# Optimization experiments

Hardware: AMD Instinct MI355X
Metric: run time of the kernel (lower is better)

The kernel has to match this reference:

```python
import jax, jax.numpy as jnp
import numpy as np

ALPHA = 1.5  # entmax alpha (EntmaxBisect default behavior, exponent 1/(alpha-1)=2)
N_ITER = 50  # EntmaxBisect default number of bisection iterations


def entmax_bisect(x, alpha=ALPHA, n_iter=N_ITER):
    """Entmax via bisection along the last axis (Peters & Martins), matching
    the torch entmax.EntmaxBisect forward (with ensure_sum_one=True)."""
    d = x.shape[-1]
    xs = x * (alpha - 1.0)
    max_val = jnp.max(xs, axis=-1, keepdims=True)
    tau_lo = max_val - 1.0
    tau_hi = max_val - (1.0 / d) ** (alpha - 1.0)

    inv_am1 = 1.0 / (alpha - 1.0)  # = 2.0 for alpha=1.5

    def p(tau):
        return jnp.maximum(xs - tau, 0.0) ** inv_am1

    f_lo = jnp.sum(p(tau_lo), axis=-1, keepdims=True) - 1.0
    dm0 = tau_hi - tau_lo

    def body(i, carry):
        tau_lo, dm = carry
        dm = dm * 0.5
        tau_m = tau_lo + dm
        f_m = jnp.sum(p(tau_m), axis=-1, keepdims=True) - 1.0
        tau_lo = jnp.where(f_m * f_lo >= 0, tau_m, tau_lo)
        return (tau_lo, dm)

    tau_lo, dm = jax.lax.fori_loop(0, n_iter, body, (tau_lo, dm0))
    p_m = p(tau_lo + dm)
    return p_m / jnp.sum(p_m, axis=-1, keepdims=True)


def setup_inputs() -> dict:
    key = jax.random.key(0)
    k1, k2, k3, k4 = jax.random.split(key, 4)
    bsz, nfield, nemb = 2048, 128, 128
    nhead, nhid, d_k = 8, 64, 64

    def xavier(k, shape, gain=1.414):
        fan_in, fan_out = shape[-2], shape[-1]
        std = gain * np.sqrt(2.0 / (fan_in + fan_out))
        return jax.random.normal(k, shape, dtype=jnp.float32) * std

    return {
        "x": jax.random.normal(k1, (bsz, nfield, nemb), dtype=jnp.float32),
        "bilinear_w": xavier(k2, (nhead, nemb, d_k)),
        "query": xavier(k3, (nhead, nhid, d_k)),
        "values": xavier(k4, (nhead, nhid, nfield)),
    }


def reference(x, bilinear_w, query, values):
    # x: [b, f, x(=nemb)]; bilinear_w: [k, x, y(=d_k)]; query: [k, o(=nhid), y]
    d_k = bilinear_w.shape[-1]
    scale = d_k ** (-0.5)
    # einsum('bfx,kxy,koy->bkof') split into two contractions
    kx = jnp.einsum('bfx,kxy->bkfy', x, bilinear_w)            # [b,k,f,y]
    att_gates = jnp.einsum('bkfy,koy->bkof', kx, query) * scale  # [b,k,o,f]
    sparse_gates = entmax_bisect(att_gates)
    return sparse_gates * values[None]  # einsum('bkof,kof->bkof')
```

## Files before the change

kernel.cpp:

```cpp
#include <hip/hip_runtime.h>
#include <hip/hip_bf16.h>


using half8_t  = __attribute__((ext_vector_type(8))) _Float16;
using half4_t  = __attribute__((ext_vector_type(4))) _Float16;
using fp16x2   = __attribute__((ext_vector_type(2))) __fp16;
using floatx4  = __attribute__((ext_vector_type(4))) float;

#define NBIS 8

#if defined(__has_builtin)
#if __has_builtin(__builtin_amdgcn_fdot2)
#define HAS_FDOT2 1
#endif
#endif
#ifndef HAS_FDOT2
#define HAS_FDOT2 0
#endif

__device__ __forceinline__ float frcp(float x) {
#if __has_builtin(__builtin_amdgcn_rcpf)
    return __builtin_amdgcn_rcpf(x);
#else
    return 1.0f / x;
#endif
}

__global__ __launch_bounds__(256) void w2_kernel(const float* __restrict__ bw,
                                                 const float* __restrict__ qm,
                                                 _Float16* __restrict__ W2h) {
    const int k  = blockIdx.x >> 3;
    const int og = blockIdx.x & 7;
    __shared__ float Lbw[128 * 65];
    __shared__ float Lq[8 * 64];
    const int t = threadIdx.x;

    const float* bwk = bw + k * 8192;
    #pragma unroll
    for (int i2 = 0; i2 < 8; ++i2) {
        int i = t + i2 * 256;
        float4 v = ((const float4*)bwk)[i];
        int xx = (i * 4) >> 6, y = (i * 4) & 63;
        float* dst = &Lbw[xx * 65 + y];
        dst[0] = v.x; dst[1] = v.y; dst[2] = v.z; dst[3] = v.w;
    }
    const float* qk = qm + k * 4096 + og * 8 * 64;
    if (t < 128) ((float4*)Lq)[t] = ((const float4*)qk)[t];
    __syncthreads();

    #pragma unroll
    for (int i = 0; i < 4; ++i) {
        int ox = i * 256 + t;
        int o = ox >> 7, x = ox & 127;
        const float* brow = &Lbw[x * 65];
        const float* qrow = &Lq[o * 64];
        float acc = 0.f;
        #pragma unroll
        for (int y = 0; y < 64; ++y) acc = fmaf(brow[y], qrow[y], acc);
        W2h[(k * 64 + og * 8 + o) * 128 + x] = (_Float16)(acc * 0.0625f);
    }
}

__global__ __launch_bounds__(256, 3) void satt_kernel(
        const float* __restrict__ xg, const _Float16* __restrict__ W2h,
        const float* __restrict__ values, float* __restrict__ out) {
    const int bid = blockIdx.x;
    const int k = (bid & 511) >> 6;
    const int b = ((bid >> 9) << 6) | (bid & 63);
    const int t = threadIdx.x;
    const int w = t >> 6, l = t & 63;

    __shared__ __align__(16) char smem[52224];
    _Float16* Ash = (_Float16*)smem;
    _Float16* Bsh = (_Float16*)(smem + 17408);
    float*    zsh = (float*)smem;

    const _Float16* w2k = W2h + k * 8192;
    #pragma unroll
    for (int j = 0; j < 4; ++j) {
        int c = t + 256 * j;
        int o = c >> 4, x0 = (c & 15) * 8;
        uint4 v = ((const uint4*)w2k)[c];
        *(uint4*)(Ash + o * 136 + x0) = v;
    }
    const float* xb = xg + (size_t)b * 16384;
    #pragma unroll
    for (int j = 0; j < 16; ++j) {
        int c = t + 256 * j;
        int f = c >> 5, x0 = (c & 31) * 4;
        float4 v = ((const float4*)xb)[c];
        half4_t h;
        h[0] = (_Float16)v.x; h[1] = (_Float16)v.y;
        h[2] = (_Float16)v.z; h[3] = (_Float16)v.w;
        *(half4_t*)(Bsh + f * 136 + x0) = h;
    }
    __syncthreads();

    const int q = l >> 4, c16 = l & 15;
    half8_t afrag[4];
    #pragma unroll
    for (int kk = 0; kk < 4; ++kk)
        afrag[kk] = *(const half8_t*)(Ash + (w * 16 + c16) * 136 + kk * 32 + q * 8);

    floatx4 acc[8];
    #pragma unroll
    for (int ft = 0; ft < 8; ++ft) acc[ft] = (floatx4){0.f, 0.f, 0.f, 0.f};

    #pragma unroll
    for (int kk = 0; kk < 4; ++kk) {
        #pragma unroll
        for (int ft = 0; ft < 8; ++ft) {
            half8_t bfrag = *(const half8_t*)(Bsh + (ft * 16 + c16) * 136 + kk * 32 + q * 8);
            acc[ft] = __builtin_amdgcn_mfma_f32_16x16x32_f16(afrag[kk], bfrag, acc[ft], 0, 0, 0);
        }
    }
    __syncthreads();

    #pragma unroll
    for (int ft = 0; ft < 8; ++ft) {
        #pragma unroll
        for (int r = 0; r < 4; ++r)
            zsh[(w * 16 + q * 4 + r) * 132 + ft * 16 + c16] = acc[ft][r];
    }
    __syncthreads();

    const int row = l >> 2, s = l & 3;
    const int o = w * 16 + row;
    float zz[32];
    #pragma unroll
    for (int j = 0; j < 8; ++j) {
        floatx4 v = *(const floatx4*)(zsh + o * 132 + s * 32 + j * 4);
        zz[4 * j + 0] = v[0]; zz[4 * j + 1] = v[1];
        zz[4 * j + 2] = v[2]; zz[4 * j + 3] = v[3];
    }
    float m0 = zz[0], m1 = zz[1], m2 = zz[2], m3 = zz[3];
    #pragma unroll
    for (int j = 4; j < 32; j += 4) {
        m0 = fmaxf(m0, zz[j + 0]); m1 = fmaxf(m1, zz[j + 1]);
        m2 = fmaxf(m2, zz[j + 2]); m3 = fmaxf(m3, zz[j + 3]);
    }
    float m = fmaxf(fmaxf(m0, m1), fmaxf(m2, m3));
    m = fmaxf(m, __shfl_xor(m, 1));
    m = fmaxf(m, __shfl_xor(m, 2));

    float tau = m - 1.0f;
    float dm  = 0.9116116523516816f;

#if HAS_FDOT2
    fp16x2 zh[16];
    #pragma unroll
    for (int j = 0; j < 16; ++j)
        zh[j] = __builtin_amdgcn_cvt_pkrtz(zz[2 * j], zz[2 * j + 1]);
    const fp16x2 hzero = { (__fp16)0.f, (__fp16)0.f };
    const fp16x2 hone  = { (__fp16)1.f, (__fp16)1.f };

    #pragma unroll
    for (int it = 0; it < NBIS; ++it) {
        dm *= 0.5f;
        float tm = tau + dm;
        fp16x2 t2 = __builtin_amdgcn_cvt_pkrtz(tm, tm);
        float sa = 0.f, sb = 0.f;
        #pragma unroll
        for (int j = 0; j < 16; j += 2) {
            fp16x2 d0 = __builtin_elementwise_max(zh[j]     - t2, hzero);
            fp16x2 d1 = __builtin_elementwise_max(zh[j + 1] - t2, hzero);
            sa = __builtin_amdgcn_fdot2(d0, d0, sa, false);
            sb = __builtin_amdgcn_fdot2(d1, d1, sb, false);
        }
        float sm = sa + sb;
        sm += __shfl_xor(sm, 1); sm += __shfl_xor(sm, 2);
        tau = (sm >= 1.0f) ? tm : tau;
    }
    #pragma unroll
    for (int it = 0; it < 2; ++it) {
        fp16x2 t2 = __builtin_amdgcn_cvt_pkrtz(tau, tau);
        float s2a = 0.f, s2b = 0.f, s1a = 0.f, s1b = 0.f;
        #pragma unroll
        for (int j = 0; j < 16; j += 2) {
            fp16x2 d0 = __builtin_elementwise_max(zh[j]     - t2, hzero);
            fp16x2 d1 = __builtin_elementwise_max(zh[j + 1] - t2, hzero);
            s2a = __builtin_amdgcn_fdot2(d0, d0, s2a, false);
            s2b = __builtin_amdgcn_fdot2(d1, d1, s2b, false);
            s1a = __builtin_amdgcn_fdot2(d0, hone, s1a, false);
            s1b = __builtin_amdgcn_fdot2(d1, hone, s1b, false);
        }
        float s2 = s2a + s2b, s1 = s1a + s1b;
        s2 += __shfl_xor(s2, 1); s2 += __shfl_xor(s2, 2);
        s1 += __shfl_xor(s1, 1); s1 += __shfl_xor(s1, 2);
        tau += (s2 - 1.0f) * frcp(fmaxf(s1 + s1, 1e-6f));
    }
#else
    #pragma unroll
    for (int it = 0; it < NBIS + 4; ++it) {
        dm *= 0.5f;
        float tm = tau + dm;
        float sa = 0.f, sb = 0.f;
        #pragma unroll
        for (int j = 0; j < 32; j += 2) {
            float d0 = fmaxf(zz[j] - tm, 0.f);
            float d1 = fmaxf(zz[j + 1] - tm, 0.f);
            sa = fmaf(d0, d0, sa); sb = fmaf(d1, d1, sb);
        }
        float sm = sa + sb;
        sm += __shfl_xor(sm, 1); sm += __shfl_xor(sm, 2);
        tau = (sm >= 1.0f) ? tm : tau;
    }
    {
        float s2a = 0.f, s2b = 0.f, s1a = 0.f, s1b = 0.f;
        #pragma unroll
        for (int j = 0; j < 32; j += 2) {
            float d0 = fmaxf(zz[j] - tau, 0.f);
            float d1 = fmaxf(zz[j + 1] - tau, 0.f);
            s2a = fmaf(d0, d0, s2a); s2b = fmaf(d1, d1, s2b);
            s1a += d0; s1b += d1;
        }
        float s2 = s2a + s2b, s1 = s1a + s1b;
        s2 += __shfl_xor(s2, 1); s2 += __shfl_xor(s2, 2);
        s1 += __shfl_xor(s1, 1); s1 += __shfl_xor(s1, 2);
        tau += (s2 - 1.0f) * frcp(fmaxf(s1 + s1, 1e-6f));
    }
#endif
    {
        float s2a = 0.f, s2b = 0.f, s1a = 0.f, s1b = 0.f;
        #pragma unroll
        for (int j = 0; j < 32; j += 2) {
            float d0 = fmaxf(zz[j] - tau, 0.f);
            float d1 = fmaxf(zz[j + 1] - tau, 0.f);
            s2a = fmaf(d0, d0, s2a); s2b = fmaf(d1, d1, s2b);
            s1a += d0; s1b += d1;
        }
        float s2 = s2a + s2b, s1 = s1a + s1b;
        s2 += __shfl_xor(s2, 1); s2 += __shfl_xor(s2, 2);
        s1 += __shfl_xor(s1, 1); s1 += __shfl_xor(s1, 2);
        tau += (s2 - 1.0f) * frcp(fmaxf(s1 + s1, 1e-6f));
    }

    float ps0 = 0.f, ps1 = 0.f;
    #pragma unroll
    for (int j = 0; j < 32; j += 2) {
        float d0 = fmaxf(zz[j] - tau, 0.f);
        float d1 = fmaxf(zz[j + 1] - tau, 0.f);
        float p0 = d0 * d0, p1 = d1 * d1;
        zz[j] = p0; zz[j + 1] = p1;
        ps0 += p0; ps1 += p1;
    }
    float ps = ps0 + ps1;
    ps += __shfl_xor(ps, 1); ps += __shfl_xor(ps, 2);
    const float inv = 1.0f / ps;

    const float* vrow = values + ((k * 64 + o) * 128 + s * 32);
    float* orow = out + ((((size_t)b * 8 + k) * 64 + o) * 128 + s * 32);
    #pragma unroll
    for (int j = 0; j < 8; ++j) {
        floatx4 vv = *(const floatx4*)(vrow + 4 * j);
        floatx4 g;
        g[0] = zz[4 * j + 0] * inv * vv[0];
        g[1] = zz[4 * j + 1] * inv * vv[1];
        g[2] = zz[4 * j + 2] * inv * vv[2];
        g[3] = zz[4 * j + 3] * inv * vv[3];
        *(floatx4*)(orow + 4 * j) = g;
    }
}

extern "C" void kernel_launch(void* const* d_in, const int* in_sizes, int n_in,
                              void* d_out, int out_size, void* d_ws, size_t ws_size,
                              hipStream_t stream) {
    const float* xg     = (const float*)d_in[0];
    const float* bw     = (const float*)d_in[1];
    const float* qm     = (const float*)d_in[2];
    const float* values = (const float*)d_in[3];
    float* out = (float*)d_out;
    _Float16* W2h = (_Float16*)d_ws;

    w2_kernel<<<64, 256, 0, stream>>>(bw, qm, W2h);
    satt_kernel<<<16384, 256, 0, stream>>>(xg, W2h, values, out);
}
```

Baseline: 816.4 us.

## Drop LDS staging: MFMA straight from global fp16 x, transposed output mapping

Removes the shared-memory staging of W2 and x and the LDS round trip for the score matrix. Operands are swapped so each lane's MFMA accumulator already holds one row's values, and the entmax reductions now use cross-lane shuffles at distance 16 and 32. When the workspace is large enough, a separate pre-pass converts x to fp16 once, halving the bytes each block reads; otherwise blocks convert fp32 x themselves. Freeing LDS lets occupancy rise to 6 blocks per CU, at the cost of an extra launch and an extra write and read of the fp16 copy of x.

```diff
diff --git a/kernel.cpp b/kernel.cpp
--- a/kernel.cpp
+++ b/kernel.cpp
@@ -61,77 +61,75 @@
     }
 }
 
-__global__ __launch_bounds__(256, 3) void satt_kernel(
-        const float* __restrict__ xg, const _Float16* __restrict__ W2h,
+__global__ __launch_bounds__(256) void xh_kernel(const float* __restrict__ xg,
+                                                 _Float16* __restrict__ xh) {
+    const size_t n4 = (size_t)2048 * 128 * 32;
+    const size_t stride = (size_t)gridDim.x * 256;
+    for (size_t i = (size_t)blockIdx.x * 256 + threadIdx.x; i < n4; i += stride) {
+        float4 v = ((const float4*)xg)[i];
+        half4_t h;
+        h[0] = (_Float16)v.x; h[1] = (_Float16)v.y;
+        h[2] = (_Float16)v.z; h[3] = (_Float16)v.w;
+        ((half4_t*)xh)[i] = h;
+    }
+}
+
+template<bool PRE>
+__global__ __launch_bounds__(256, 6) void satt_kernel(
+        const float* __restrict__ xg, const _Float16* __restrict__ Xh,
+        const _Float16* __restrict__ W2h,
         const float* __restrict__ values, float* __restrict__ out) {
     const int bid = blockIdx.x;
     const int k = (bid & 511) >> 6;
     const int b = ((bid >> 9) << 6) | (bid & 63);
     const int t = threadIdx.x;
     const int w = t >> 6, l = t & 63;
-
-    __shared__ __align__(16) char smem[52224];
-    _Float16* Ash = (_Float16*)smem;
-    _Float16* Bsh = (_Float16*)(smem + 17408);
-    float*    zsh = (float*)smem;
-
-    const _Float16* w2k = W2h + k * 8192;
-    #pragma unroll
-    for (int j = 0; j < 4; ++j) {
-        int c = t + 256 * j;
-        int o = c >> 4, x0 = (c & 15) * 8;
-        uint4 v = ((const uint4*)w2k)[c];
-        *(uint4*)(Ash + o * 136 + x0) = v;
-    }
-    const float* xb = xg + (size_t)b * 16384;
-    #pragma unroll
-    for (int j = 0; j < 16; ++j) {
-        int c = t + 256 * j;
-        int f = c >> 5, x0 = (c & 31) * 4;
-        float4 v = ((const float4*)xb)[c];
-        half4_t h;
-        h[0] = (_Float16)v.x; h[1] = (_Float16)v.y;
-        h[2] = (_Float16)v.z; h[3] = (_Float16)v.w;
-        *(half4_t*)(Bsh + f * 136 + x0) = h;
-    }
-    __syncthreads();
-
     const int q = l >> 4, c16 = l & 15;
-    half8_t afrag[4];
+    const int o = w * 16 + c16;
+
+    half8_t bfrag[4];
+    const _Float16* w2row = W2h + ((k * 64 + o) << 7);
     #pragma unroll
     for (int kk = 0; kk < 4; ++kk)
-        afrag[kk] = *(const half8_t*)(Ash + (w * 16 + c16) * 136 + kk * 32 + q * 8);
+        bfrag[kk] = *(const half8_t*)(w2row + kk * 32 + q * 8);
 
     floatx4 acc[8];
     #pragma unroll
-    for (int ft = 0; ft < 8; ++ft) acc[ft] = (floatx4){0.f, 0.f, 0.f, 0.f};
-
-    #pragma unroll
-    for (int kk = 0; kk < 4; ++kk) {
-        #pragma unroll
-        for (int ft = 0; ft < 8; ++ft) {
-            half8_t bfrag = *(const half8_t*)(Bsh + (ft * 16 + c16) * 136 + kk * 32 + q * 8);
-            acc[ft] = __builtin_amdgcn_mfma_f32_16x16x32_f16(afrag[kk], bfrag, acc[ft], 0, 0, 0);
-        }
-    }
-    __syncthreads();
-
-    #pragma unroll
-    for (int ft = 0; ft < 8; ++ft) {
-        #pragma unroll
-        for (int r = 0; r < 4; ++r)
-            zsh[(w * 16 + q * 4 + r) * 132 + ft * 16 + c16] = acc[ft][r];
-    }
-    __syncthreads();
-
-    const int row = l >> 2, s = l & 3;
-    const int o = w * 16 + row;
+    for (int mt = 0; mt < 8; ++mt) acc[mt] = (floatx4){0.f, 0.f, 0.f, 0.f};
+
+    if (PRE) {
+        const _Float16* xb = Xh + (size_t)b * 16384;
+        #pragma unroll
+        for (int kk = 0; kk < 4; ++kk) {
+            #pragma unroll
+            for (int mt = 0; mt < 8; ++mt) {
+                half8_t a = *(const half8_t*)(xb + (mt * 16 + c16) * 128 + kk * 32 + q * 8);
+                acc[mt] = __builtin_amdgcn_mfma_f32_16x16x32_f16(a, bfrag[kk], acc[mt], 0, 0, 0);
+            }
+        }
+    } else {
+        const float* xb = xg + (size_t)b * 16384;
+        #pragma unroll
+        for (int kk = 0; kk < 4; ++kk) {
+            #pragma unroll
+            for (int mt = 0; mt < 8; ++mt) {
+                const float4* p = (const float4*)(xb + (mt * 16 + c16) * 128 + kk * 32 + q * 8);
+                float4 v0 = p[0], v1 = p[1];
+                half8_t a;
+                a[0] = (_Float16)v0.x; a[1] = (_Float16)v0.y;
+                a[2] = (_Float16)v0.z; a[3] = (_Float16)v0.w;
+                a[4] = (_Float16)v1.x; a[5] = (_Float16)v1.y;
+                a[6] = (_Float16)v1.z; a[7] = (_Float16)v1.w;
+                acc[mt] = __builtin_amdgcn_mfma_f32_16x16x32_f16(a, bfrag[kk], acc[mt], 0, 0, 0);
+            }
+        }
+    }
+
     float zz[32];
     #pragma unroll
-    for (int j = 0; j < 8; ++j) {
-        floatx4 v = *(const floatx4*)(zsh + o * 132 + s * 32 + j * 4);
-        zz[4 * j + 0] = v[0]; zz[4 * j + 1] = v[1];
-        zz[4 * j + 2] = v[2]; zz[4 * j + 3] = v[3];
+    for (int mt = 0; mt < 8; ++mt) {
+        zz[4 * mt + 0] = acc[mt][0]; zz[4 * mt + 1] = acc[mt][1];
+        zz[4 * mt + 2] = acc[mt][2]; zz[4 * mt + 3] = acc[mt][3];
     }
     float m0 = zz[0], m1 = zz[1], m2 = zz[2], m3 = zz[3];
     #pragma unroll
@@ -140,8 +138,8 @@
         m2 = fmaxf(m2, zz[j + 2]); m3 = fmaxf(m3, zz[j + 3]);
     }
     float m = fmaxf(fmaxf(m0, m1), fmaxf(m2, m3));
-    m = fmaxf(m, __shfl_xor(m, 1));
-    m = fmaxf(m, __shfl_xor(m, 2));
+    m = fmaxf(m, __shfl_xor(m, 16));
+    m = fmaxf(m, __shfl_xor(m, 32));
 
     float tau = m - 1.0f;
     float dm  = 0.9116116523516816f;
@@ -168,7 +166,7 @@
             sb = __builtin_amdgcn_fdot2(d1, d1, sb, false);
         }
         float sm = sa + sb;
-        sm += __shfl_xor(sm, 1); sm += __shfl_xor(sm, 2);
+        sm += __shfl_xor(sm, 16); sm += __shfl_xor(sm, 32);
         tau = (sm >= 1.0f) ? tm : tau;
     }
     #pragma unroll
@@ -185,8 +183,8 @@
             s1b = __builtin_amdgcn_fdot2(d1, hone, s1b, false);
         }
         float s2 = s2a + s2b, s1 = s1a + s1b;
-        s2 += __shfl_xor(s2, 1); s2 += __shfl_xor(s2, 2);
-        s1 += __shfl_xor(s1, 1); s1 += __shfl_xor(s1, 2);
+        s2 += __shfl_xor(s2, 16); s2 += __shfl_xor(s2, 32);
+        s1 += __shfl_xor(s1, 16); s1 += __shfl_xor(s1, 32);
         tau += (s2 - 1.0f) * frcp(fmaxf(s1 + s1, 1e-6f));
     }
 #else
@@ -202,7 +200,7 @@
             sa = fmaf(d0, d0, sa); sb = fmaf(d1, d1, sb);
         }
         float sm = sa + sb;
-        sm += __shfl_xor(sm, 1); sm += __shfl_xor(sm, 2);
+        sm += __shfl_xor(sm, 16); sm += __shfl_xor(sm, 32);
         tau = (sm >= 1.0f) ? tm : tau;
     }
     {
@@ -215,8 +213,8 @@
             s1a += d0; s1b += d1;
         }
         float s2 = s2a + s2b, s1 = s1a + s1b;
-        s2 += __shfl_xor(s2, 1); s2 += __shfl_xor(s2, 2);
-        s1 += __shfl_xor(s1, 1); s1 += __shfl_xor(s1, 2);
+        s2 += __shfl_xor(s2, 16); s2 += __shfl_xor(s2, 32);
+        s1 += __shfl_xor(s1, 16); s1 += __shfl_xor(s1, 32);
         tau += (s2 - 1.0f) * frcp(fmaxf(s1 + s1, 1e-6f));
     }
 #endif
@@ -230,8 +228,8 @@
             s1a += d0; s1b += d1;
         }
         float s2 = s2a + s2b, s1 = s1a + s1b;
-        s2 += __shfl_xor(s2, 1); s2 += __shfl_xor(s2, 2);
-        s1 += __shfl_xor(s1, 1); s1 += __shfl_xor(s1, 2);
+        s2 += __shfl_xor(s2, 16); s2 += __shfl_xor(s2, 32);
+        s1 += __shfl_xor(s1, 16); s1 += __shfl_xor(s1, 32);
         tau += (s2 - 1.0f) * frcp(fmaxf(s1 + s1, 1e-6f));
     }
 
@@ -245,20 +243,20 @@
         ps0 += p0; ps1 += p1;
     }
     float ps = ps0 + ps1;
-    ps += __shfl_xor(ps, 1); ps += __shfl_xor(ps, 2);
+    ps += __shfl_xor(ps, 16); ps += __shfl_xor(ps, 32);
     const float inv = 1.0f / ps;
 
-    const float* vrow = values + ((k * 64 + o) * 128 + s * 32);
-    float* orow = out + ((((size_t)b * 8 + k) * 64 + o) * 128 + s * 32);
-    #pragma unroll
-    for (int j = 0; j < 8; ++j) {
-        floatx4 vv = *(const floatx4*)(vrow + 4 * j);
+    const float* vrow = values + ((k * 64 + o) << 7) + q * 4;
+    float* orow = out + ((((size_t)b * 8 + k) * 64 + o) << 7) + q * 4;
+    #pragma unroll
+    for (int mt = 0; mt < 8; ++mt) {
+        floatx4 vv = *(const floatx4*)(vrow + mt * 16);
         floatx4 g;
-        g[0] = zz[4 * j + 0] * inv * vv[0];
-        g[1] = zz[4 * j + 1] * inv * vv[1];
-        g[2] = zz[4 * j + 2] * inv * vv[2];
-        g[3] = zz[4 * j + 3] * inv * vv[3];
-        *(floatx4*)(orow + 4 * j) = g;
+        g[0] = zz[4 * mt + 0] * inv * vv[0];
+        g[1] = zz[4 * mt + 1] * inv * vv[1];
+        g[2] = zz[4 * mt + 2] * inv * vv[2];
+        g[3] = zz[4 * mt + 3] * inv * vv[3];
+        *(floatx4*)(orow + mt * 16) = g;
     }
 }
 
@@ -271,7 +269,15 @@
     const float* values = (const float*)d_in[3];
     float* out = (float*)d_out;
     _Float16* W2h = (_Float16*)d_ws;
+    _Float16* Xh  = (_Float16*)((char*)d_ws + 131072);
+
+    const size_t need = 131072 + (size_t)2048 * 128 * 128 * 2;
 
     w2_kernel<<<64, 256, 0, stream>>>(bw, qm, W2h);
-    satt_kernel<<<16384, 256, 0, stream>>>(xg, W2h, values, out);
-}
+    if (ws_size >= need) {
+        xh_kernel<<<8192, 256, 0, stream>>>(xg, Xh);
+        satt_kernel<true><<<16384, 256, 0, stream>>>(xg, Xh, W2h, values, out);
+    } else {
+        satt_kernel<false><<<16384, 256, 0, stream>>>(xg, Xh, W2h, values, out);
+    }
+}
```

Measured after the change: 906.6 us. 1.11x slower.
